# Optimization experiments

Measured on AMD Instinct MI355X. Metric: run time of the kernel, lower is better.

The kernel has to match this reference:

```python
import jax, jax.numpy as jnp
import numpy as np

B, L, C, H = 4, 2048, 1024, 16
D = C // H
MAX_SCALE_MUL = float(np.log(100.0))
EPS = 1e-12


def setup_inputs() -> dict:
    key = jax.random.key(0)
    ks = jax.random.split(key, 7)
    return {
        "x": jax.random.normal(ks[0], (B, L, C), dtype=jnp.float32),
        "W_qkv": jax.random.normal(ks[1], (3 * C, C), dtype=jnp.float32) * (C ** -0.5),
        "q_bias": jax.random.normal(ks[2], (C,), dtype=jnp.float32) * 0.02,
        "v_bias": jax.random.normal(ks[3], (C,), dtype=jnp.float32) * 0.02,
        "scale_mul_log": jnp.full((1, H, 1, 1), np.log(4.0), dtype=jnp.float32),
        "W_proj": jax.random.normal(ks[4], (C, C), dtype=jnp.float32) * (C ** -0.5),
        "b_proj": jax.random.normal(ks[5], (C,), dtype=jnp.float32) * 0.02,
    }


def reference(x, W_qkv, q_bias, v_bias, scale_mul_log, W_proj, b_proj):
    Bb, Ll, Cc = x.shape
    # fused QKV projection with bias = cat(q_bias, zeros, v_bias)
    bias = jnp.concatenate([q_bias, jnp.zeros_like(q_bias), v_bias])
    qkv = (x @ W_qkv.T + bias).reshape(Bb, Ll, 3, H, D)
    q, k, v = (jnp.transpose(qkv[:, :, i], (0, 2, 1, 3)) for i in range(3))  # [B,H,L,D]
    # L2-norm attention: normalize q,k; learned per-head scale on q (clamped)
    scale_mul = jnp.exp(jnp.minimum(scale_mul_log, MAX_SCALE_MUL))  # [1,H,1,1]
    q = q / jnp.maximum(jnp.linalg.norm(q, axis=-1, keepdims=True), EPS) * scale_mul
    k = k / jnp.maximum(jnp.linalg.norm(k, axis=-1, keepdims=True), EPS)
    # SDPA with scale=1 (attn_l2_norm path), no mask, no dropout (eval)
    scores = jnp.einsum("bhqd,bhkd->bhqk", q, k)
    attn = jax.nn.softmax(scores, axis=-1)
    out = jnp.einsum("bhqk,bhkd->bhqd", attn, v)
    out = jnp.transpose(out, (0, 2, 1, 3)).reshape(Bb, Ll, Cc)
    return out @ W_proj.T + b_proj
```

## Files before the change

### kernel.cpp

```cpp
#include <hip/hip_runtime.h>
#include <hip/hip_bf16.h>


typedef __attribute__((ext_vector_type(8))) short bf16x8;
typedef __attribute__((ext_vector_type(4))) float f32x4;
typedef __attribute__((ext_vector_type(16))) float f32x16;

#define MAXLOG 4.60517018598809f
#define LOG2E  1.4426950408889634f

__device__ __forceinline__ float bf2f(unsigned short u) {
    union { unsigned int i; float f; } v; v.i = ((unsigned int)u) << 16; return v.f;
}
__device__ __forceinline__ unsigned short f2bf(float f) {
    union { float f; unsigned int i; } v; v.f = f;
    unsigned int x = v.i;
    return (unsigned short)((x + 0x7FFFu + ((x >> 16) & 1u)) >> 16);
}
__device__ __forceinline__ unsigned fbits(float f) {
    union { float f; unsigned u; } v; v.f = f; return v.u;
}
__device__ __forceinline__ bf16x8 pack8(const float* __restrict__ p) {
    float4 a = *(const float4*)p;
    float4 b = *(const float4*)(p + 4);
    bf16x8 r;
    r[0] = (short)f2bf(a.x); r[1] = (short)f2bf(a.y);
    r[2] = (short)f2bf(a.z); r[3] = (short)f2bf(a.w);
    r[4] = (short)f2bf(b.x); r[5] = (short)f2bf(b.y);
    r[6] = (short)f2bf(b.z); r[7] = (short)f2bf(b.w);
    return r;
}
__device__ __forceinline__ void gload_lds16(const void* g, void* l) {
    __builtin_amdgcn_global_load_lds((const __attribute__((address_space(1))) void*)g,
                                     (__attribute__((address_space(3))) void*)l, 16, 0, 0);
}

__global__ __launch_bounds__(256) void k_cast_bf16(const float* __restrict__ src,
                                                   unsigned short* __restrict__ dst, int n8) {
    int i = blockIdx.x * 256 + threadIdx.x;
    if (i < n8) *(bf16x8*)&dst[(long)i * 8] = pack8(&src[(long)i * 8]);
}

__global__ void k_build_bias(const float* __restrict__ qb, const float* __restrict__ vb,
                             float* __restrict__ bias3) {
    int i = blockIdx.x * 256 + threadIdx.x;
    if (i < 3072) {
        float v = 0.0f;
        if (i < 1024) v = qb[i];
        else if (i >= 2048) v = vb[i - 2048];
        bias3[i] = v;
    }
}

template<bool B_F32, bool OUT_F32>
__global__ __launch_bounds__(256) void k_gemm_lds(
    const unsigned short* __restrict__ A, const void* __restrict__ Bp,
    const float* __restrict__ bias, void* __restrict__ Cp, int N, int K)
{
    __shared__ unsigned short As[128 * 32];
    __shared__ unsigned short Bs[128 * 32];
    const int t = threadIdx.x, wave = t >> 6, lane = t & 63;
    const int quad = lane >> 4, l16 = lane & 15;
    const int bm = blockIdx.x * 128, bn = blockIdx.y * 128;
    const int wr = (wave >> 1) * 64, wc = (wave & 1) * 64;
    f32x4 acc[4][4] = {};

    const int srow = lane >> 2;
    const int scol = (lane & 3) * 8;
    const int c0 = wave * 2, c1 = wave * 2 + 1;
    const long ga0 = (long)(bm + c0 * 16 + srow) * K + scol;
    const long ga1 = (long)(bm + c1 * 16 + srow) * K + scol;
    const int sr = t >> 2, sc2 = (t & 3) * 8;
    const float* Bf = (const float*)Bp;
    const unsigned short* Bh = (const unsigned short*)Bp;
    const long gb0 = B_F32 ? ((long)(bn + sr) * K + sc2)      : ((long)(bn + c0 * 16 + srow) * K + scol);
    const long gb1 = B_F32 ? ((long)(bn + sr + 64) * K + sc2) : ((long)(bn + c1 * 16 + srow) * K + scol);

    for (int kt = 0; kt < K; kt += 32) {
        __syncthreads();
        gload_lds16(&A[ga0 + kt], &As[c0 * 512]);
        gload_lds16(&A[ga1 + kt], &As[c1 * 512]);
        if (B_F32) {
            *(bf16x8*)&Bs[sr * 32 + sc2]        = pack8(&Bf[gb0 + kt]);
            *(bf16x8*)&Bs[(sr + 64) * 32 + sc2] = pack8(&Bf[gb1 + kt]);
        } else {
            gload_lds16(&Bh[gb0 + kt], &Bs[c0 * 512]);
            gload_lds16(&Bh[gb1 + kt], &Bs[c1 * 512]);
        }
        __syncthreads();
        bf16x8 af[4], bfr[4];
        for (int i = 0; i < 4; ++i)
            af[i] = *(const bf16x8*)&As[(wr + i * 16 + l16) * 32 + quad * 8];
        for (int j = 0; j < 4; ++j)
            bfr[j] = *(const bf16x8*)&Bs[(wc + j * 16 + l16) * 32 + quad * 8];
        for (int i = 0; i < 4; ++i)
            for (int j = 0; j < 4; ++j)
                acc[i][j] = __builtin_amdgcn_mfma_f32_16x16x32_bf16(af[i], bfr[j], acc[i][j], 0, 0, 0);
    }
    for (int j = 0; j < 4; ++j) {
        int gn = bn + wc + j * 16 + l16;
        float bv = bias[gn];
        for (int i = 0; i < 4; ++i) {
            int gm0 = bm + wr + i * 16 + quad * 4;
            for (int r = 0; r < 4; ++r) {
                float val = acc[i][j][r] + bv;
                if (OUT_F32) ((float*)Cp)[(long)(gm0 + r) * N + gn] = val;
                else ((unsigned short*)Cp)[(long)(gm0 + r) * N + gn] = f2bf(val);
            }
        }
    }
}

__global__ __launch_bounds__(256) void k_norm_k(
    const unsigned short* __restrict__ qkv, unsigned short* __restrict__ kb)
{
    const int wid = blockIdx.x * 4 + (threadIdx.x >> 6);
    const int lane = threadIdx.x & 63;
    const int h = wid & 15, m = wid >> 4;
    const int b = m >> 11, l = m & 2047;
    float kv = bf2f(qkv[(long)m * 3072 + 1024 + h * 64 + lane]);
    float sk = kv * kv;
    for (int s = 32; s; s >>= 1) sk += __shfl_xor(sk, s, 64);
    float kn = kv / fmaxf(sqrtf(sk), 1e-12f);
    kb[((long)(b * 16 + h) * 2048 + l) * 64 + lane] = f2bf(kn);
}

__global__ __launch_bounds__(256) void k_vtrans(
    const unsigned short* __restrict__ qkv, unsigned short* __restrict__ vT)
{
    __shared__ unsigned short Vsh[64 * 72];
    const int t = threadIdx.x;
    const int bh = blockIdx.y, l0 = blockIdx.x * 64;
    const int h = bh & 15, b = bh >> 4;
    const int ll = t >> 2, d0 = (t & 3) * 16;
    long src = (long)(b * 2048 + l0 + ll) * 3072 + 2048 + h * 64 + d0;
    *(bf16x8*)&Vsh[ll * 72 + d0]     = *(const bf16x8*)&qkv[src];
    *(bf16x8*)&Vsh[ll * 72 + d0 + 8] = *(const bf16x8*)&qkv[src + 8];
    __syncthreads();
    const int d = t >> 2, ls = (t & 3) * 16;
    unsigned short tmp[16];
    for (int j = 0; j < 16; ++j) tmp[j] = Vsh[(ls + j) * 72 + d];
    long dst = (long)(bh * 64 + d) * 2048 + l0 + ls;
    *(bf16x8*)&vT[dst]     = *(bf16x8*)&tmp[0];
    *(bf16x8*)&vT[dst + 8] = *(bf16x8*)&tmp[8];
}

__global__ __launch_bounds__(256, 3) void k_attn32(
    const unsigned short* __restrict__ qkv, const unsigned short* __restrict__ kb,
    const unsigned short* __restrict__ vT, const float* __restrict__ sml,
    unsigned short* __restrict__ attn)
{
    __shared__ unsigned short Ks[2][64 * 72];
    __shared__ unsigned short Vs[2][64 * 72];
    const int t = threadIdx.x, wave = t >> 6, lane = t & 63;
    const int m32 = lane & 31, half = lane >> 5;
    const int bh = blockIdx.y, h = bh & 15, b = bh >> 4;
    const int q0 = blockIdx.x * 128 + wave * 32;
    const float scale = __expf(fminf(sml[h], MAXLOG));
    const float c2 = scale * LOG2E;

    const int qd = m32 >> 2, lo = qd & 3;
    const int prow = ((((lo == 1) || (lo == 2)) ? (qd ^ 3) : qd) << 2) | (m32 & 3);

    bf16x8 aq[4];
    {
        long base = (long)(b * 2048 + q0 + m32) * 3072 + h * 64;
        float e[32]; float ss = 0.f;
        for (int f = 0; f < 4; ++f) {
            aq[f] = *(const bf16x8*)&qkv[base + f * 16 + half * 8];
            for (int j = 0; j < 8; ++j) { float x = bf2f((unsigned short)aq[f][j]); e[f * 8 + j] = x; ss += x * x; }
        }
        ss += __shfl_xor(ss, 32, 64);
        float rs = scale / fmaxf(sqrtf(ss), 1e-12f);
        for (int f = 0; f < 4; ++f)
            for (int j = 0; j < 8; ++j) aq[f][j] = (short)f2bf(e[f * 8 + j] * rs);
    }

    f32x16 o0 = {}, o1 = {};
    float ps0 = 0.f, ps1 = 0.f;
    const int sr = t >> 2, sc = (t & 3) * 16;
    const long kbase = (long)bh * 2048 * 64;
    const long vbase = (long)bh * 64 * 2048;

#define LOADT(kt) \
    kpA = *(const bf16x8*)&kb[kbase + (long)((kt) + sr) * 64 + sc];      \
    kpB = *(const bf16x8*)&kb[kbase + (long)((kt) + sr) * 64 + sc + 8];  \
    vpA = *(const bf16x8*)&vT[vbase + (long)sr * 2048 + (kt) + sc];      \
    vpB = *(const bf16x8*)&vT[vbase + (long)sr * 2048 + (kt) + sc + 8];

#define STORET(buf) \
    *(bf16x8*)&Ks[buf][sr * 72 + sc]     = kpA;  \
    *(bf16x8*)&Ks[buf][sr * 72 + sc + 8] = kpB;  \
    *(bf16x8*)&Vs[buf][sr * 72 + sc]     = vpA;  \
    *(bf16x8*)&Vs[buf][sr * 72 + sc + 8] = vpB;

#define ATTN_STEP(KS, VS) \
    for (int ktile = 0; ktile < 2; ++ktile) {                                             \
        f32x16 s = {};                                                                    \
        for (int f = 0; f < 4; ++f) {                                                     \
            bf16x8 bk = *(const bf16x8*)&KS[(ktile * 32 + prow) * 72 + f * 16 + half * 8];\
            s = __builtin_amdgcn_mfma_f32_32x32x16_bf16(bk, aq[f], s, 0, 0, 0);           \
        }                                                                                 \
        unsigned pu[16];                                                                  \
        for (int j = 0; j < 8; ++j) {                                                     \
            float ea = __builtin_amdgcn_exp2f(s[j] * LOG2E - c2);                         \
            float eb = __builtin_amdgcn_exp2f(s[8 + j] * LOG2E - c2);                     \
            ps0 += ea; ps1 += eb;                                                         \
            pu[j] = fbits(ea) + 0x8000u; pu[8 + j] = fbits(eb) + 0x8000u;                 \
        }                                                                                 \
        uint4 a0u, a1u;                                                                   \
        a0u.x = __builtin_amdgcn_perm(pu[1],  pu[0],  0x07060302u);                       \
        a0u.y = __builtin_amdgcn_perm(pu[3],  pu[2],  0x07060302u);                       \
        a0u.z = __builtin_amdgcn_perm(pu[5],  pu[4],  0x07060302u);                       \
        a0u.w = __builtin_amdgcn_perm(pu[7],  pu[6],  0x07060302u);                       \
        a1u.x = __builtin_amdgcn_perm(pu[9],  pu[8],  0x07060302u);                       \
        a1u.y = __builtin_amdgcn_perm(pu[11], pu[10], 0x07060302u);                       \
        a1u.z = __builtin_amdgcn_perm(pu[13], pu[12], 0x07060302u);                       \
        a1u.w = __builtin_amdgcn_perm(pu[15], pu[14], 0x07060302u);                       \
        bf16x8 ap0, ap1;                                                                  \
        __builtin_memcpy(&ap0, &a0u, 16); __builtin_memcpy(&ap1, &a1u, 16);               \
        for (int c = 0; c < 2; ++c) {                                                     \
            bf16x8 apc = c ? ap1 : ap0;                                                   \
            bf16x8 bv0 = *(const bf16x8*)&VS[m32 * 72        + ktile * 32 + c * 16 + half * 8]; \
            bf16x8 bv1 = *(const bf16x8*)&VS[(32 + m32) * 72 + ktile * 32 + c * 16 + half * 8]; \
            o0 = __builtin_amdgcn_mfma_f32_32x32x16_bf16(apc, bv0, o0, 0, 0, 0);          \
            o1 = __builtin_amdgcn_mfma_f32_32x32x16_bf16(apc, bv1, o1, 0, 0, 0);          \
        }                                                                                 \
    }

    bf16x8 kpA, kpB, vpA, vpB;
    LOADT(0)
    STORET(0)
    __syncthreads();

    for (int kt = 0; kt < 2048; kt += 128) {
        LOADT(kt + 64)
        ATTN_STEP(Ks[0], Vs[0])
        STORET(1)
        __syncthreads();
        const bool more = (kt + 128) < 2048;
        if (more) { LOADT(kt + 128) }
        ATTN_STEP(Ks[1], Vs[1])
        if (more) {
            STORET(0)
            __syncthreads();
        }
    }
#undef LOADT
#undef STORET
#undef ATTN_STEP

    float fl = ps0 + ps1;
    fl += __shfl_xor(fl, 32, 64);
    for (int r = 0; r < 16; ++r) {
        int m = (r & 3) + 8 * (r >> 2) + 4 * half;
        float inv = 1.0f / __shfl(fl, m, 64);
        long dst = (long)(b * 2048 + q0 + m) * 1024 + h * 64;
        attn[dst + m32]      = f2bf(o0[r] * inv);
        attn[dst + 32 + m32] = f2bf(o1[r] * inv);
    }
}

extern "C" void kernel_launch(void* const* d_in, const int* in_sizes, int n_in,
                              void* d_out, int out_size, void* d_ws, size_t ws_size,
                              hipStream_t stream) {
    const float* x    = (const float*)d_in[0];
    const float* Wqkv = (const float*)d_in[1];
    const float* qbia = (const float*)d_in[2];
    const float* vbia = (const float*)d_in[3];
    const float* sml  = (const float*)d_in[4];
    const float* Wp   = (const float*)d_in[5];
    const float* bp   = (const float*)d_in[6];

    char* ws = (char*)d_ws;
    unsigned short* qkv   = (unsigned short*)ws;
    unsigned short* Wpb   = (unsigned short*)ws;
    unsigned short* kbuf  = (unsigned short*)(ws + 50331648);
    unsigned short* Wqkvb = kbuf;
    unsigned short* vT    = (unsigned short*)(ws + 67108864);
    unsigned short* xb    = vT;
    unsigned short* attn  = (unsigned short*)(ws + 83886080);
    float*          bias3 = (float*)(ws + 100663296);
    float*          out   = (float*)d_out;

    hipLaunchKernelGGL(k_cast_bf16, dim3(4096), dim3(256), 0, stream, x, xb, 1048576);
    hipLaunchKernelGGL(k_cast_bf16, dim3(1536), dim3(256), 0, stream, Wqkv, Wqkvb, 393216);
    hipLaunchKernelGGL(k_build_bias, dim3(12), dim3(256), 0, stream, qbia, vbia, bias3);
    hipLaunchKernelGGL((k_gemm_lds<false, false>), dim3(64, 24), dim3(256), 0, stream,
                       xb, (const void*)Wqkvb, bias3, (void*)qkv, 3072, 1024);
    hipLaunchKernelGGL(k_norm_k, dim3(32768), dim3(256), 0, stream, qkv, kbuf);
    hipLaunchKernelGGL(k_vtrans, dim3(32, 64), dim3(256), 0, stream, qkv, vT);
    hipLaunchKernelGGL(k_attn32, dim3(16, 64), dim3(256), 0, stream, qkv, kbuf, vT, sml, attn);
    hipLaunchKernelGGL(k_cast_bf16, dim3(512), dim3(256), 0, stream, Wp, Wpb, 131072);
    hipLaunchKernelGGL((k_gemm_lds<false, true>), dim3(64, 8), dim3(256), 0, stream,
                       attn, (const void*)Wpb, bp, (void*)out, 1024, 1024);
}
```

Measured before the change: 321.8 us.

## Fuse prep kernels, compute softmax denominator via MFMA, raise attention occupancy

Merges the input/weight casts and bias construction into one kernel, and merges K normalisation with V transpose into one kernel reading each qkv row once. The attention kernel computes row sums with an extra MFMA against a ones vector instead of scalar VALU adds, and its launch bound is raised to 4 blocks per CU. This reduces launch count and memory passes and removes VALU reduction work, at the cost of extra MFMA work and possible register pressure or spills.

```diff
diff --git a/kernel.cpp b/kernel.cpp
--- a/kernel.cpp
+++ b/kernel.cpp
@@ -35,26 +35,37 @@
                                      (__attribute__((address_space(3))) void*)l, 16, 0, 0);
 }
 
-__global__ __launch_bounds__(256) void k_cast_bf16(const float* __restrict__ src,
-                                                   unsigned short* __restrict__ dst, int n8) {
+__global__ __launch_bounds__(256) void k_prep(
+    const float* __restrict__ x, const float* __restrict__ Wqkv,
+    const float* __restrict__ Wp, const float* __restrict__ qbia,
+    const float* __restrict__ vbia,
+    unsigned short* __restrict__ xb, unsigned short* __restrict__ Wqkvb,
+    unsigned short* __restrict__ Wpb, float* __restrict__ bias3)
+{
     int i = blockIdx.x * 256 + threadIdx.x;
-    if (i < n8) *(bf16x8*)&dst[(long)i * 8] = pack8(&src[(long)i * 8]);
-}
-
-__global__ void k_build_bias(const float* __restrict__ qb, const float* __restrict__ vb,
-                             float* __restrict__ bias3) {
-    int i = blockIdx.x * 256 + threadIdx.x;
-    if (i < 3072) {
-        float v = 0.0f;
-        if (i < 1024) v = qb[i];
-        else if (i >= 2048) v = vb[i - 2048];
-        bias3[i] = v;
-    }
-}
-
-template<bool B_F32, bool OUT_F32>
+    if (i < 1048576) {
+        *(bf16x8*)&xb[(long)i * 8] = pack8(&x[(long)i * 8]);
+    } else if (i < 1441792) {
+        int j = i - 1048576;
+        *(bf16x8*)&Wqkvb[(long)j * 8] = pack8(&Wqkv[(long)j * 8]);
+    } else if (i < 1572864) {
+        int j = i - 1441792;
+        *(bf16x8*)&Wpb[(long)j * 8] = pack8(&Wp[(long)j * 8]);
+    } else if (i < 1573248) {
+        int j = (i - 1572864) * 8;
+        for (int u = 0; u < 8; ++u) {
+            int n = j + u;
+            float v = 0.0f;
+            if (n < 1024) v = qbia[n];
+            else if (n >= 2048) v = vbia[n - 2048];
+            bias3[n] = v;
+        }
+    }
+}
+
+template<bool OUT_F32>
 __global__ __launch_bounds__(256) void k_gemm_lds(
-    const unsigned short* __restrict__ A, const void* __restrict__ Bp,
+    const unsigned short* __restrict__ A, const unsigned short* __restrict__ Bh,
     const float* __restrict__ bias, void* __restrict__ Cp, int N, int K)
 {
     __shared__ unsigned short As[128 * 32];
@@ -70,23 +81,15 @@
     const int c0 = wave * 2, c1 = wave * 2 + 1;
     const long ga0 = (long)(bm + c0 * 16 + srow) * K + scol;
     const long ga1 = (long)(bm + c1 * 16 + srow) * K + scol;
-    const int sr = t >> 2, sc2 = (t & 3) * 8;
-    const float* Bf = (const float*)Bp;
-    const unsigned short* Bh = (const unsigned short*)Bp;
-    const long gb0 = B_F32 ? ((long)(bn + sr) * K + sc2)      : ((long)(bn + c0 * 16 + srow) * K + scol);
-    const long gb1 = B_F32 ? ((long)(bn + sr + 64) * K + sc2) : ((long)(bn + c1 * 16 + srow) * K + scol);
+    const long gb0 = (long)(bn + c0 * 16 + srow) * K + scol;
+    const long gb1 = (long)(bn + c1 * 16 + srow) * K + scol;
 
     for (int kt = 0; kt < K; kt += 32) {
         __syncthreads();
         gload_lds16(&A[ga0 + kt], &As[c0 * 512]);
         gload_lds16(&A[ga1 + kt], &As[c1 * 512]);
-        if (B_F32) {
-            *(bf16x8*)&Bs[sr * 32 + sc2]        = pack8(&Bf[gb0 + kt]);
-            *(bf16x8*)&Bs[(sr + 64) * 32 + sc2] = pack8(&Bf[gb1 + kt]);
-        } else {
-            gload_lds16(&Bh[gb0 + kt], &Bs[c0 * 512]);
-            gload_lds16(&Bh[gb1 + kt], &Bs[c1 * 512]);
-        }
+        gload_lds16(&Bh[gb0 + kt], &Bs[c0 * 512]);
+        gload_lds16(&Bh[gb1 + kt], &Bs[c1 * 512]);
         __syncthreads();
         bf16x8 af[4], bfr[4];
         for (int i = 0; i < 4; ++i)
@@ -111,31 +114,35 @@
     }
 }
 
-__global__ __launch_bounds__(256) void k_norm_k(
-    const unsigned short* __restrict__ qkv, unsigned short* __restrict__ kb)
-{
-    const int wid = blockIdx.x * 4 + (threadIdx.x >> 6);
-    const int lane = threadIdx.x & 63;
-    const int h = wid & 15, m = wid >> 4;
-    const int b = m >> 11, l = m & 2047;
-    float kv = bf2f(qkv[(long)m * 3072 + 1024 + h * 64 + lane]);
-    float sk = kv * kv;
-    for (int s = 32; s; s >>= 1) sk += __shfl_xor(sk, s, 64);
-    float kn = kv / fmaxf(sqrtf(sk), 1e-12f);
-    kb[((long)(b * 16 + h) * 2048 + l) * 64 + lane] = f2bf(kn);
-}
-
-__global__ __launch_bounds__(256) void k_vtrans(
-    const unsigned short* __restrict__ qkv, unsigned short* __restrict__ vT)
+__global__ __launch_bounds__(256) void k_prep_kv(
+    const unsigned short* __restrict__ qkv, unsigned short* __restrict__ kb,
+    unsigned short* __restrict__ vT)
 {
     __shared__ unsigned short Vsh[64 * 72];
     const int t = threadIdx.x;
     const int bh = blockIdx.y, l0 = blockIdx.x * 64;
     const int h = bh & 15, b = bh >> 4;
-    const int ll = t >> 2, d0 = (t & 3) * 16;
-    long src = (long)(b * 2048 + l0 + ll) * 3072 + 2048 + h * 64 + d0;
-    *(bf16x8*)&Vsh[ll * 72 + d0]     = *(const bf16x8*)&qkv[src];
-    *(bf16x8*)&Vsh[ll * 72 + d0 + 8] = *(const bf16x8*)&qkv[src + 8];
+    const int ll = t >> 2, c16 = (t & 3) * 16;
+    const long rowbase = (long)(b * 2048 + l0 + ll) * 3072;
+
+    {
+        bf16x8 k0 = *(const bf16x8*)&qkv[rowbase + 1024 + h * 64 + c16];
+        bf16x8 k1 = *(const bf16x8*)&qkv[rowbase + 1024 + h * 64 + c16 + 8];
+        float e[16]; float ss = 0.f;
+        for (int j = 0; j < 8; ++j) { e[j]     = bf2f((unsigned short)k0[j]); ss += e[j] * e[j]; }
+        for (int j = 0; j < 8; ++j) { e[8 + j] = bf2f((unsigned short)k1[j]); ss += e[8 + j] * e[8 + j]; }
+        ss += __shfl_xor(ss, 1, 64);
+        ss += __shfl_xor(ss, 2, 64);
+        float rs = 1.0f / fmaxf(sqrtf(ss), 1e-12f);
+        bf16x8 o0, o1;
+        for (int j = 0; j < 8; ++j) o0[j] = (short)f2bf(e[j] * rs);
+        for (int j = 0; j < 8; ++j) o1[j] = (short)f2bf(e[8 + j] * rs);
+        long dst = ((long)bh * 2048 + l0 + ll) * 64 + c16;
+        *(bf16x8*)&kb[dst]     = o0;
+        *(bf16x8*)&kb[dst + 8] = o1;
+    }
+    *(bf16x8*)&Vsh[ll * 72 + c16]     = *(const bf16x8*)&qkv[rowbase + 2048 + h * 64 + c16];
+    *(bf16x8*)&Vsh[ll * 72 + c16 + 8] = *(const bf16x8*)&qkv[rowbase + 2048 + h * 64 + c16 + 8];
     __syncthreads();
     const int d = t >> 2, ls = (t & 3) * 16;
     unsigned short tmp[16];
@@ -145,7 +152,7 @@
     *(bf16x8*)&vT[dst + 8] = *(bf16x8*)&tmp[8];
 }
 
-__global__ __launch_bounds__(256, 3) void k_attn32(
+__global__ __launch_bounds__(256, 4) void k_attn32(
     const unsigned short* __restrict__ qkv, const unsigned short* __restrict__ kb,
     const unsigned short* __restrict__ vT, const float* __restrict__ sml,
     unsigned short* __restrict__ attn)
@@ -176,8 +183,8 @@
             for (int j = 0; j < 8; ++j) aq[f][j] = (short)f2bf(e[f * 8 + j] * rs);
     }
 
-    f32x16 o0 = {}, o1 = {};
-    float ps0 = 0.f, ps1 = 0.f;
+    f32x16 o0 = {}, o1 = {}, lacc = {};
+    bf16x8 ones; for (int i = 0; i < 8; ++i) ones[i] = (short)0x3F80;
     const int sr = t >> 2, sc = (t & 3) * 16;
     const long kbase = (long)bh * 2048 * 64;
     const long vbase = (long)bh * 64 * 2048;
@@ -203,10 +210,8 @@
         }                                                                                 \
         unsigned pu[16];                                                                  \
         for (int j = 0; j < 8; ++j) {                                                     \
-            float ea = __builtin_amdgcn_exp2f(s[j] * LOG2E - c2);                         \
-            float eb = __builtin_amdgcn_exp2f(s[8 + j] * LOG2E - c2);                     \
-            ps0 += ea; ps1 += eb;                                                         \
-            pu[j] = fbits(ea) + 0x8000u; pu[8 + j] = fbits(eb) + 0x8000u;                 \
+            pu[j]     = fbits(__builtin_amdgcn_exp2f(s[j]     * LOG2E - c2));             \
+            pu[8 + j] = fbits(__builtin_amdgcn_exp2f(s[8 + j] * LOG2E - c2));             \
         }                                                                                 \
         uint4 a0u, a1u;                                                                   \
         a0u.x = __builtin_amdgcn_perm(pu[1],  pu[0],  0x07060302u);                       \
@@ -223,8 +228,9 @@
             bf16x8 apc = c ? ap1 : ap0;                                                   \
             bf16x8 bv0 = *(const bf16x8*)&VS[m32 * 72        + ktile * 32 + c * 16 + half * 8]; \
             bf16x8 bv1 = *(const bf16x8*)&VS[(32 + m32) * 72 + ktile * 32 + c * 16 + half * 8]; \
-            o0 = __builtin_amdgcn_mfma_f32_32x32x16_bf16(apc, bv0, o0, 0, 0, 0);          \
-            o1 = __builtin_amdgcn_mfma_f32_32x32x16_bf16(apc, bv1, o1, 0, 0, 0);          \
+            o0   = __builtin_amdgcn_mfma_f32_32x32x16_bf16(apc, bv0, o0, 0, 0, 0);        \
+            o1   = __builtin_amdgcn_mfma_f32_32x32x16_bf16(apc, bv1, o1, 0, 0, 0);        \
+            lacc = __builtin_amdgcn_mfma_f32_32x32x16_bf16(apc, ones, lacc, 0, 0, 0);     \
         }                                                                                 \
     }
 
@@ -250,11 +256,9 @@
 #undef STORET
 #undef ATTN_STEP
 
-    float fl = ps0 + ps1;
-    fl += __shfl_xor(fl, 32, 64);
     for (int r = 0; r < 16; ++r) {
         int m = (r & 3) + 8 * (r >> 2) + 4 * half;
-        float inv = 1.0f / __shfl(fl, m, 64);
+        float inv = 1.0f / lacc[r];
         long dst = (long)(b * 2048 + q0 + m) * 1024 + h * 64;
         attn[dst + m32]      = f2bf(o0[r] * inv);
         attn[dst + 32 + m32] = f2bf(o1[r] * inv);
@@ -274,24 +278,21 @@
 
     char* ws = (char*)d_ws;
     unsigned short* qkv   = (unsigned short*)ws;
-    unsigned short* Wpb   = (unsigned short*)ws;
     unsigned short* kbuf  = (unsigned short*)(ws + 50331648);
     unsigned short* Wqkvb = kbuf;
     unsigned short* vT    = (unsigned short*)(ws + 67108864);
     unsigned short* xb    = vT;
-    unsigned short* attn  = (unsigned short*)(ws + 83886080);
+    unsigned short* attnb = (unsigned short*)(ws + 83886080);
     float*          bias3 = (float*)(ws + 100663296);
+    unsigned short* Wpb   = (unsigned short*)(ws + 100679680);
     float*          out   = (float*)d_out;
 
-    hipLaunchKernelGGL(k_cast_bf16, dim3(4096), dim3(256), 0, stream, x, xb, 1048576);
-    hipLaunchKernelGGL(k_cast_bf16, dim3(1536), dim3(256), 0, stream, Wqkv, Wqkvb, 393216);
-    hipLaunchKernelGGL(k_build_bias, dim3(12), dim3(256), 0, stream, qbia, vbia, bias3);
-    hipLaunchKernelGGL((k_gemm_lds<false, false>), dim3(64, 24), dim3(256), 0, stream,
-                       xb, (const void*)Wqkvb, bias3, (void*)qkv, 3072, 1024);
-    hipLaunchKernelGGL(k_norm_k, dim3(32768), dim3(256), 0, stream, qkv, kbuf);
-    hipLaunchKernelGGL(k_vtrans, dim3(32, 64), dim3(256), 0, stream, qkv, vT);
-    hipLaunchKernelGGL(k_attn32, dim3(16, 64), dim3(256), 0, stream, qkv, kbuf, vT, sml, attn);
-    hipLaunchKernelGGL(k_cast_bf16, dim3(512), dim3(256), 0, stream, Wp, Wpb, 131072);
-    hipLaunchKernelGGL((k_gemm_lds<false, true>), dim3(64, 8), dim3(256), 0, stream,
-                       attn, (const void*)Wpb, bp, (void*)out, 1024, 1024);
-}
+    hipLaunchKernelGGL(k_prep, dim3(6146), dim3(256), 0, stream,
+                       x, Wqkv, Wp, qbia, vbia, xb, Wqkvb, Wpb, bias3);
+    hipLaunchKernelGGL((k_gemm_lds<false>), dim3(64, 24), dim3(256), 0, stream,
+                       xb, Wqkvb, bias3, (void*)qkv, 3072, 1024);
+    hipLaunchKernelGGL(k_prep_kv, dim3(32, 64), dim3(256), 0, stream, qkv, kbuf, vT);
+    hipLaunchKernelGGL(k_attn32, dim3(16, 64), dim3(256), 0, stream, qkv, kbuf, vT, sml, attnb);
+    hipLaunchKernelGGL((k_gemm_lds<true>), dim3(64, 8), dim3(256), 0, stream,
+                       attnb, Wpb, bp, (void*)out, 1024, 1024);
+}
```

After: 299.0 us. 1.08x faster.
